# Kernel tuning notes

Measured on AMD Instinct MI355X. Metric: run time of the kernel, lower is better.

The kernel has to match this reference:

```python
import jax, jax.numpy as jnp
import numpy as np

P = 512       # input_shape
HD = 256      # hidden_dim
N = 65536     # number of samples
LAM1 = 1.0
LAM3 = 1.0


def setup_inputs() -> dict:
    key = jax.random.key(0)
    ks = jax.random.split(key, 12)
    def lin(kw, kb, out_d, in_d):
        lim = 1.0 / np.sqrt(in_d)
        W = jax.random.uniform(kw, (out_d, in_d), jnp.float32, -lim, lim)
        b = jax.random.uniform(kb, (out_d,), jnp.float32, -lim, lim)
        return W, b
    W1, b1 = lin(ks[0], ks[1], 200, P + HD)
    W12, b12 = lin(ks[2], ks[3], 100, 200)
    W13, b13 = lin(ks[4], ks[5], 100, 100)
    W2, b2 = lin(ks[6], ks[7], P, 100)
    return {
        "input": jax.random.normal(ks[8], (N, P), jnp.float32),
        "h": jax.random.normal(ks[9], (N, HD), jnp.float32),
        "W1": W1, "b1": b1, "W12": W12, "b12": b12,
        "W13": W13, "b13": b13, "W2": W2, "b2": b2,
        "idx0": 0, "idx1": N,
    }


def reference(input, h, W1, b1, W12, b12, W13, b13, W2, b2, idx0, idx1):
    n = input.shape[0]
    hs = h[idx0:idx1]                                   # [N, HD]
    x = jnp.concatenate([input, hs], axis=1)            # [N, P+HD]
    x = jax.nn.relu(x @ W1.T + b1)                      # dropout = identity (eval)
    x = jax.nn.relu(x @ W12.T + b12)
    x = jax.nn.relu(x @ W13.T + b13)
    f_x_h = x @ W2.T + b2                               # [N, P]
    mu = jnp.mean(hs, axis=0)                           # [HD]
    # S = mean_i <h_i, h_i> : vectorized sum-of-squares (replaces Python loop)
    S = jnp.mean(jnp.sum(hs * hs, axis=1))
    part0 = jnp.linalg.norm(f_x_h[:-1] - input[1:]) / (n - 1)
    part1 = LAM1 * jnp.sum(jnp.abs(mu)) / HD
    part2 = LAM1 * jnp.abs(S / HD - 1.0)
    part3 = LAM3 * jnp.mean(jnp.sum(jnp.abs(hs[1:] - hs[:-1]), axis=1)) / HD
    return (f_x_h, part0, part1, part2, part3)
```

## Files before the change

### kernel.cpp

```cpp
#include <hip/hip_runtime.h>

typedef __bf16 bf16;
typedef __bf16 bf16x8 __attribute__((ext_vector_type(8)));
typedef float f32x4 __attribute__((ext_vector_type(4)));

#define N_ROWS 65536

#define W1_E   159744
#define W12_E  25088
#define W13_E  14336
#define W2_E   65536
#define WP_TOTAL (W1_E + W12_E + W13_E + W2_E)
#define W12_OFF_B 319488
#define W13_OFF_B 369664
#define W2_OFF_B  398336
#define BP_OFF_BYTES (WP_TOTAL * 2)
#define BP_FLOATS 944
#define ACC_OFF_BYTES (BP_OFF_BYTES + BP_FLOATS * 4)
#define NCOPY 16
#define ACC_FLOATS (NCOPY * 256 + 3)
#define P0_IDX (NCOPY * 256)
#define S_IDX  (NCOPY * 256 + 1)
#define P3_IDX (NCOPY * 256 + 2)

__device__ inline int swz4(int r) { return (r ^ (r >> 2)) & 3; }

__global__ void pack_kernel(const float* __restrict__ W1, const float* __restrict__ b1,
                            const float* __restrict__ W12, const float* __restrict__ b12,
                            const float* __restrict__ W13, const float* __restrict__ b13,
                            const float* __restrict__ W2, const float* __restrict__ b2,
                            bf16* __restrict__ wp, float* __restrict__ bp) {
  int i = blockIdx.x * 256 + threadIdx.x;
  if (i < WP_TOTAL) {
    float v = 0.0f;
    if (i < W1_E) {
      int s = i / 6656, b = i - s * 6656;
      int r = b >> 5, w = b & 31;
      int k = s * 32 + (((w >> 3) ^ swz4(r)) << 3) + (w & 7);
      if (r < 200) v = W1[r * 768 + k];
    } else if (i < W1_E + W12_E) {
      int j = i - W1_E;
      int s = j / 3584, b = j - s * 3584;
      int r = b >> 5, w = b & 31;
      int k = s * 32 + (((w >> 3) ^ swz4(r)) << 3) + (w & 7);
      if (r < 100 && k < 200) v = W12[r * 200 + k];
    } else if (i < W1_E + W12_E + W13_E) {
      int j = i - (W1_E + W12_E);
      int s = j / 3584, b = j - s * 3584;
      int r = b >> 5, w = b & 31;
      int k = s * 32 + (((w >> 3) ^ swz4(r)) << 3) + (w & 7);
      if (r < 100 && k < 100) v = W13[r * 100 + k];
    } else {
      int j = i - (W1_E + W12_E + W13_E);
      int g = j >> 14, rest = j & 16383;
      int s = rest >> 12, b = rest & 4095;
      int r = b >> 5, w = b & 31;
      int o = g * 128 + r;
      int k = s * 32 + (((w >> 3) ^ swz4(r)) << 3) + (w & 7);
      if (k < 100) v = W2[o * 100 + k];
    }
    wp[i] = (bf16)v;
  } else {
    int j = i - WP_TOTAL;
    if (j < BP_FLOATS) {
      float v = 0.0f;
      if (j < 208)      { if (j < 200) v = b1[j]; }
      else if (j < 320) { int o = j - 208; if (o < 100) v = b12[o]; }
      else if (j < 432) { int o = j - 320; if (o < 100) v = b13[o]; }
      else              { v = b2[j - 432]; }
      bp[j] = v;
    }
  }
}

#define MFMA(a, b, c) __builtin_amdgcn_mfma_f32_16x16x32_bf16((a), (b), (c), 0, 0, 0)

template<int BYTES>
__device__ inline void stage(const char* __restrict__ src, bf16* __restrict__ dstw, int tid) {
  char* dst = (char*)dstw;
  const int off0 = (tid >> 6) * 1024 + (tid & 63) * 16;
  constexpr int NCH = (BYTES + 4095) / 4096;
#pragma unroll
  for (int j = 0; j < NCH; j++) {
    const int off = j * 4096 + off0;
    if ((BYTES & 4095) == 0 || off < BYTES)
      __builtin_amdgcn_global_load_lds(
          (const __attribute__((address_space(1))) void*)(src + off),
          (__attribute__((address_space(3))) void*)(dst + off),
          16, 0, 0);
  }
}

__global__ __launch_bounds__(256, 2) void mlp_main(
    const float* __restrict__ input, const float* __restrict__ h,
    const bf16* __restrict__ wp, const float* __restrict__ bp,
    float* __restrict__ out, float* __restrict__ p0_accum) {
  __shared__ __align__(16) bf16 acts[4][3712];
  __shared__ __align__(16) bf16 wbuf[2][6656];
  __shared__ float p0red[4];

  const int tid = threadIdx.x;
  const int lane = tid & 63;
  const int wave = tid >> 6;
  const int c16 = lane & 15;
  const int quad = lane >> 4;
  const int m0 = blockIdx.x * 64 + wave * 16;
  const int qs8 = (quad ^ swz4(c16)) * 8;

  const char* wpb = (const char*)wp;
  const float* b1p  = bp;
  const float* b12p = bp + 208;
  const float* b13p = bp + 320;
  const float* b2p  = bp + 432;

  bf16* actw = &acts[wave][0];

  f32x4 acc1[13];
#pragma unroll
  for (int t = 0; t < 13; t++) acc1[t] = (f32x4){0.f, 0.f, 0.f, 0.f};

  stage<13312>(wpb, wbuf[0], tid);
  __syncthreads();

  const float* arow = input + (size_t)(m0 + c16) * 512 + quad * 8;
  const float* hrow = h + (size_t)(m0 + c16) * 256 + quad * 8;
  f32x4 abuf[16];
  for (int kb = 0; kb < 3; kb++) {
#pragma unroll
    for (int b = 0; b < 8; b++) {
      const int kk = kb * 8 + b;
      const float* p = (kk < 16) ? (arow + kk * 32) : (hrow + (kk - 16) * 32);
      abuf[b * 2]     = *(const f32x4*)p;
      abuf[b * 2 + 1] = *(const f32x4*)(p + 4);
    }
#pragma unroll
    for (int b = 0; b < 8; b++) {
      const int ks = kb * 8 + b;
      if (ks + 1 < 24) stage<13312>(wpb + (ks + 1) * 13312, wbuf[(b + 1) & 1], tid);
      bf16x8 a;
#pragma unroll
      for (int q = 0; q < 4; q++) { a[q] = (bf16)abuf[b * 2][q]; a[4 + q] = (bf16)abuf[b * 2 + 1][q]; }
      const bf16* buf = wbuf[b & 1];
#pragma unroll
      for (int t = 0; t < 13; t++) {
        bf16x8 bb = *(const bf16x8*)(buf + (t * 16 + c16) * 32 + qs8);
        acc1[t] = MFMA(a, bb, acc1[t]);
      }
      __syncthreads();
    }
  }
#pragma unroll
  for (int t = 0; t < 13; t++) {
    const float bias = b1p[t * 16 + c16];
#pragma unroll
    for (int r = 0; r < 4; r++)
      actw[(quad * 4 + r) * 232 + t * 16 + c16] = (bf16)fmaxf(acc1[t][r] + bias, 0.0f);
  }
  for (int idx = lane; idx < 256; idx += 64)
    actw[(idx >> 4) * 232 + 208 + (idx & 15)] = (bf16)0.0f;

  f32x4 acc2[7];
#pragma unroll
  for (int t = 0; t < 7; t++) acc2[t] = (f32x4){0.f, 0.f, 0.f, 0.f};

  stage<7168>(wpb + W12_OFF_B, wbuf[0], tid);
  __syncthreads();
#pragma unroll
  for (int ks = 0; ks < 7; ks++) {
    if (ks + 1 < 7) stage<7168>(wpb + W12_OFF_B + (ks + 1) * 7168, wbuf[(ks + 1) & 1], tid);
    bf16x8 a = *(const bf16x8*)(actw + c16 * 232 + ks * 32 + quad * 8);
    const bf16* buf = wbuf[ks & 1];
#pragma unroll
    for (int t = 0; t < 7; t++) {
      bf16x8 bb = *(const bf16x8*)(buf + (t * 16 + c16) * 32 + qs8);
      acc2[t] = MFMA(a, bb, acc2[t]);
    }
    __syncthreads();
  }
#pragma unroll
  for (int t = 0; t < 7; t++) {
    const float bias = b12p[t * 16 + c16];
#pragma unroll
    for (int r = 0; r < 4; r++)
      actw[(quad * 4 + r) * 136 + t * 16 + c16] = (bf16)fmaxf(acc2[t][r] + bias, 0.0f);
  }
  for (int idx = lane; idx < 256; idx += 64)
    actw[(idx >> 4) * 136 + 112 + (idx & 15)] = (bf16)0.0f;

  f32x4 acc3[7];
#pragma unroll
  for (int t = 0; t < 7; t++) acc3[t] = (f32x4){0.f, 0.f, 0.f, 0.f};

  stage<7168>(wpb + W13_OFF_B, wbuf[0], tid);
  __syncthreads();
#pragma unroll
  for (int ks = 0; ks < 4; ks++) {
    if (ks + 1 < 4) stage<7168>(wpb + W13_OFF_B + (ks + 1) * 7168, wbuf[(ks + 1) & 1], tid);
    bf16x8 a = *(const bf16x8*)(actw + c16 * 136 + ks * 32 + quad * 8);
    const bf16* buf = wbuf[ks & 1];
#pragma unroll
    for (int t = 0; t < 7; t++) {
      bf16x8 bb = *(const bf16x8*)(buf + (t * 16 + c16) * 32 + qs8);
      acc3[t] = MFMA(a, bb, acc3[t]);
    }
    __syncthreads();
  }
#pragma unroll
  for (int t = 0; t < 7; t++) {
    const float bias = b13p[t * 16 + c16];
#pragma unroll
    for (int r = 0; r < 4; r++)
      actw[(quad * 4 + r) * 136 + t * 16 + c16] = (bf16)fmaxf(acc3[t][r] + bias, 0.0f);
  }
  for (int idx = lane; idx < 256; idx += 64)
    actw[(idx >> 4) * 136 + 112 + (idx & 15)] = (bf16)0.0f;

  float p0local = 0.0f;
  for (int g = 0; g < 4; g++) {
    f32x4 acc4[8];
#pragma unroll
    for (int t = 0; t < 8; t++) acc4[t] = (f32x4){0.f, 0.f, 0.f, 0.f};

    const char* Wg = wpb + W2_OFF_B + g * 32768;
    stage<8192>(Wg, wbuf[0], tid);
    __syncthreads();
#pragma unroll
    for (int ks = 0; ks < 4; ks++) {
      if (ks + 1 < 4) stage<8192>(Wg + (ks + 1) * 8192, wbuf[(ks + 1) & 1], tid);
      bf16x8 a = *(const bf16x8*)(actw + c16 * 136 + ks * 32 + quad * 8);
      const bf16* buf = wbuf[ks & 1];
#pragma unroll
      for (int t = 0; t < 8; t++) {
        bf16x8 bb = *(const bf16x8*)(buf + (t * 16 + c16) * 32 + qs8);
        acc4[t] = MFMA(a, bb, acc4[t]);
      }
      __syncthreads();
    }
#pragma unroll
    for (int t = 0; t < 8; t++) {
      const int o = g * 128 + t * 16 + c16;
      const float bias = b2p[o];
#pragma unroll
      for (int r = 0; r < 4; r++) {
        const int grow = m0 + quad * 4 + r;
        float v = acc4[t][r] + bias;
        out[(size_t)grow * 512 + o] = v;
        if (grow < N_ROWS - 1) {
          float d = v - input[(size_t)(grow + 1) * 512 + o];
          p0local += d * d;
        }
      }
    }
  }
#pragma unroll
  for (int off = 32; off > 0; off >>= 1) p0local += __shfl_down(p0local, off);
  if (lane == 0) p0red[wave] = p0local;
  __syncthreads();
  if (tid == 0) atomicAdd(p0_accum, p0red[0] + p0red[1] + p0red[2] + p0red[3]);
}

__global__ __launch_bounds__(256) void reduce_h(const float* __restrict__ h, float* __restrict__ acc) {
  __shared__ f32x4 cbuf[256];
  __shared__ float redS[256];
  __shared__ float redP[256];
  const int t = threadIdx.x;
  const int c = t & 63;
  const int rg = t >> 6;
  const int start = blockIdx.x * 256 + rg * 64;

  const float* base = h + (size_t)start * 256 + c * 4;
  f32x4 prev = *(const f32x4*)base;
  f32x4 csum = prev;
  f32x4 s2v = prev * prev;
  f32x4 p3v = (f32x4){0.f, 0.f, 0.f, 0.f};
#pragma unroll 8
  for (int r = 1; r < 64; r++) {
    f32x4 v = *(const f32x4*)(base + (size_t)r * 256);
    csum += v;
    s2v += v * v;
    f32x4 d = v - prev;
#pragma unroll
    for (int i = 0; i < 4; i++) p3v[i] += __builtin_fabsf(d[i]);
    prev = v;
  }
  if (start + 64 < N_ROWS) {
    f32x4 v = *(const f32x4*)(base + (size_t)64 * 256);
    f32x4 d = v - prev;
#pragma unroll
    for (int i = 0; i < 4; i++) p3v[i] += __builtin_fabsf(d[i]);
  }
  cbuf[t] = csum;
  redS[t] = s2v[0] + s2v[1] + s2v[2] + s2v[3];
  redP[t] = p3v[0] + p3v[1] + p3v[2] + p3v[3];
  __syncthreads();
  if (rg == 0) {
    f32x4 s = cbuf[c] + cbuf[c + 64] + cbuf[c + 128] + cbuf[c + 192];
    float* dst = acc + (blockIdx.x & (NCOPY - 1)) * 256 + 4 * c;
    atomicAdd(dst + 0, s[0]);
    atomicAdd(dst + 1, s[1]);
    atomicAdd(dst + 2, s[2]);
    atomicAdd(dst + 3, s[3]);
  }
  for (int st = 128; st > 0; st >>= 1) {
    if (t < st) { redS[t] += redS[t + st]; redP[t] += redP[t + st]; }
    __syncthreads();
  }
  if (t == 0) {
    atomicAdd(&acc[S_IDX], redS[0]);
    atomicAdd(&acc[P3_IDX], redP[0]);
  }
}

__global__ void finalize(const float* __restrict__ acc, float* __restrict__ out) {
  __shared__ float red[256];
  const int t = threadIdx.x;
  float s = 0.0f;
#pragma unroll
  for (int j = 0; j < NCOPY; j++) s += acc[j * 256 + t];
  red[t] = fabsf(s);
  __syncthreads();
  for (int st = 128; st > 0; st >>= 1) {
    if (t < st) red[t] += red[t + st];
    __syncthreads();
  }
  if (t == 0) {
    out[(size_t)N_ROWS * 512 + 0] = sqrtf(acc[P0_IDX]) / 65535.0f;
    out[(size_t)N_ROWS * 512 + 1] = red[0] / 65536.0f / 256.0f;
    out[(size_t)N_ROWS * 512 + 2] = fabsf(acc[S_IDX] / (65536.0f * 256.0f) - 1.0f);
    out[(size_t)N_ROWS * 512 + 3] = acc[P3_IDX] / (65535.0f * 256.0f);
  }
}

extern "C" void kernel_launch(void* const* d_in, const int* in_sizes, int n_in,
                              void* d_out, int out_size, void* d_ws, size_t ws_size,
                              hipStream_t stream) {
  const float* input = (const float*)d_in[0];
  const float* h   = (const float*)d_in[1];
  const float* W1  = (const float*)d_in[2];
  const float* b1  = (const float*)d_in[3];
  const float* W12 = (const float*)d_in[4];
  const float* b12 = (const float*)d_in[5];
  const float* W13 = (const float*)d_in[6];
  const float* b13 = (const float*)d_in[7];
  const float* W2  = (const float*)d_in[8];
  const float* b2  = (const float*)d_in[9];
  float* out = (float*)d_out;

  bf16* wp = (bf16*)d_ws;
  float* bp = (float*)((char*)d_ws + BP_OFF_BYTES);
  float* acc = (float*)((char*)d_ws + ACC_OFF_BYTES);

  hipMemsetAsync(acc, 0, ACC_FLOATS * sizeof(float), stream);
  pack_kernel<<<(WP_TOTAL + BP_FLOATS + 255) / 256, 256, 0, stream>>>(
      W1, b1, W12, b12, W13, b13, W2, b2, wp, bp);
  mlp_main<<<N_ROWS / 64, 256, 0, stream>>>(input, h, wp, bp, out, acc + P0_IDX);
  reduce_h<<<N_ROWS / 256, 256, 0, stream>>>(h, acc);
  finalize<<<1, 256, 0, stream>>>(acc, out);
}
```

Measured before the change: 412.9 us.

## Coalesce A-tile loads via LDS staging and widen h-reduction parallelism

In the MLP kernel, each wave now loads its 16 input/h rows with coalesced 128-column float4 reads, converts them to bf16, and writes them into a swizzled per-wave LDS buffer. MFMA operands are then read from that buffer, and the next chunk is prefetched into registers. This replaces the old per-lane strided 32-byte reads straight from global memory. The h statistics reduction now launches 8x more blocks, each covering 8 rows per thread, and the scalar S/P3 atomics are spread across 16 copies to cut contention. The cost is 16 KB of extra LDS per block, which may affect occupancy, plus more atomics overall.

```diff
diff --git a/kernel.cpp b/kernel.cpp
--- a/kernel.cpp
+++ b/kernel.cpp
@@ -1,6 +1,7 @@
 #include <hip/hip_runtime.h>
 
 typedef __bf16 bf16;
+typedef __bf16 bf16x4 __attribute__((ext_vector_type(4)));
 typedef __bf16 bf16x8 __attribute__((ext_vector_type(8)));
 typedef float f32x4 __attribute__((ext_vector_type(4)));
 
@@ -18,10 +19,10 @@
 #define BP_FLOATS 944
 #define ACC_OFF_BYTES (BP_OFF_BYTES + BP_FLOATS * 4)
 #define NCOPY 16
-#define ACC_FLOATS (NCOPY * 256 + 3)
 #define P0_IDX (NCOPY * 256)
-#define S_IDX  (NCOPY * 256 + 1)
-#define P3_IDX (NCOPY * 256 + 2)
+#define S_IDX0 (P0_IDX + 1)
+#define P3_IDX0 (S_IDX0 + NCOPY)
+#define ACC_FLOATS (P3_IDX0 + NCOPY)
 
 __device__ inline int swz4(int r) { return (r ^ (r >> 2)) & 3; }
 
@@ -97,6 +98,7 @@
     float* __restrict__ out, float* __restrict__ p0_accum) {
   __shared__ __align__(16) bf16 acts[4][3712];
   __shared__ __align__(16) bf16 wbuf[2][6656];
+  __shared__ __align__(16) bf16 abuf[4][2048];
   __shared__ float p0red[4];
 
   const int tid = threadIdx.x;
@@ -114,33 +116,51 @@
   const float* b2p  = bp + 432;
 
   bf16* actw = &acts[wave][0];
+  bf16* aw = &abuf[wave][0];
 
   f32x4 acc1[13];
 #pragma unroll
   for (int t = 0; t < 13; t++) acc1[t] = (f32x4){0.f, 0.f, 0.f, 0.f};
 
+  f32x4 ar[8];
+  auto loadA = [&](int kb) {
+#pragma unroll
+    for (int i = 0; i < 8; i++) {
+      const int row = 2 * i + (lane >> 5);
+      const int col = (lane & 31) * 4;
+      const float* src = (kb < 4)
+          ? (input + (size_t)(m0 + row) * 512 + kb * 128 + col)
+          : (h + (size_t)(m0 + row) * 256 + (kb - 4) * 128 + col);
+      ar[i] = *(const f32x4*)src;
+    }
+  };
+  auto writeA = [&]() {
+    const int kk = (lane & 31) >> 3;
+    const int q  = ((lane & 31) >> 1) & 3;
+    const int sub = (lane & 1) * 4;
+#pragma unroll
+    for (int i = 0; i < 8; i++) {
+      const int row = 2 * i + (lane >> 5);
+      bf16x4 cv;
+#pragma unroll
+      for (int c = 0; c < 4; c++) cv[c] = (bf16)ar[i][c];
+      *(bf16x4*)(aw + kk * 512 + row * 32 + ((q ^ swz4(row)) * 8) + sub) = cv;
+    }
+  };
+
   stage<13312>(wpb, wbuf[0], tid);
-  __syncthreads();
-
-  const float* arow = input + (size_t)(m0 + c16) * 512 + quad * 8;
-  const float* hrow = h + (size_t)(m0 + c16) * 256 + quad * 8;
-  f32x4 abuf[16];
-  for (int kb = 0; kb < 3; kb++) {
-#pragma unroll
-    for (int b = 0; b < 8; b++) {
-      const int kk = kb * 8 + b;
-      const float* p = (kk < 16) ? (arow + kk * 32) : (hrow + (kk - 16) * 32);
-      abuf[b * 2]     = *(const f32x4*)p;
-      abuf[b * 2 + 1] = *(const f32x4*)(p + 4);
-    }
-#pragma unroll
-    for (int b = 0; b < 8; b++) {
-      const int ks = kb * 8 + b;
-      if (ks + 1 < 24) stage<13312>(wpb + (ks + 1) * 13312, wbuf[(b + 1) & 1], tid);
-      bf16x8 a;
-#pragma unroll
-      for (int q = 0; q < 4; q++) { a[q] = (bf16)abuf[b * 2][q]; a[4 + q] = (bf16)abuf[b * 2 + 1][q]; }
-      const bf16* buf = wbuf[b & 1];
+  loadA(0);
+
+  for (int kb = 0; kb < 6; kb++) {
+    writeA();
+    __syncthreads();
+#pragma unroll
+    for (int j = 0; j < 4; j++) {
+      const int ks = kb * 4 + j;
+      if (j == 0 && kb + 1 < 6) loadA(kb + 1);
+      if (ks + 1 < 24) stage<13312>(wpb + (ks + 1) * 13312, wbuf[(ks + 1) & 1], tid);
+      bf16x8 a = *(const bf16x8*)(aw + j * 512 + c16 * 32 + qs8);
+      const bf16* buf = wbuf[ks & 1];
 #pragma unroll
       for (int t = 0; t < 13; t++) {
         bf16x8 bb = *(const bf16x8*)(buf + (t * 16 + c16) * 32 + qs8);
@@ -266,26 +286,23 @@
   const int t = threadIdx.x;
   const int c = t & 63;
   const int rg = t >> 6;
-  const int start = blockIdx.x * 256 + rg * 64;
+  const int start = blockIdx.x * 32 + rg * 8;
 
   const float* base = h + (size_t)start * 256 + c * 4;
-  f32x4 prev = *(const f32x4*)base;
-  f32x4 csum = prev;
-  f32x4 s2v = prev * prev;
-  f32x4 p3v = (f32x4){0.f, 0.f, 0.f, 0.f};
-#pragma unroll 8
-  for (int r = 1; r < 64; r++) {
-    f32x4 v = *(const f32x4*)(base + (size_t)r * 256);
-    csum += v;
-    s2v += v * v;
-    f32x4 d = v - prev;
-#pragma unroll
-    for (int i = 0; i < 4; i++) p3v[i] += __builtin_fabsf(d[i]);
-    prev = v;
-  }
-  if (start + 64 < N_ROWS) {
-    f32x4 v = *(const f32x4*)(base + (size_t)64 * 256);
-    f32x4 d = v - prev;
+  f32x4 v[9];
+#pragma unroll
+  for (int r = 0; r < 8; r++) v[r] = *(const f32x4*)(base + (size_t)r * 256);
+  if (start + 8 < N_ROWS) v[8] = *(const f32x4*)(base + (size_t)8 * 256);
+  else                    v[8] = v[7];
+
+  f32x4 csum = (f32x4){0.f, 0.f, 0.f, 0.f};
+  f32x4 s2v  = (f32x4){0.f, 0.f, 0.f, 0.f};
+  f32x4 p3v  = (f32x4){0.f, 0.f, 0.f, 0.f};
+#pragma unroll
+  for (int r = 0; r < 8; r++) {
+    csum += v[r];
+    s2v  += v[r] * v[r];
+    f32x4 d = v[r + 1] - v[r];
 #pragma unroll
     for (int i = 0; i < 4; i++) p3v[i] += __builtin_fabsf(d[i]);
   }
@@ -306,8 +323,8 @@
     __syncthreads();
   }
   if (t == 0) {
-    atomicAdd(&acc[S_IDX], redS[0]);
-    atomicAdd(&acc[P3_IDX], redP[0]);
+    atomicAdd(&acc[S_IDX0 + (blockIdx.x & (NCOPY - 1))], redS[0]);
+    atomicAdd(&acc[P3_IDX0 + (blockIdx.x & (NCOPY - 1))], redP[0]);
   }
 }
 
@@ -324,10 +341,13 @@
     __syncthreads();
   }
   if (t == 0) {
+    float Ssum = 0.f, Psum = 0.f;
+#pragma unroll
+    for (int j = 0; j < NCOPY; j++) { Ssum += acc[S_IDX0 + j]; Psum += acc[P3_IDX0 + j]; }
     out[(size_t)N_ROWS * 512 + 0] = sqrtf(acc[P0_IDX]) / 65535.0f;
     out[(size_t)N_ROWS * 512 + 1] = red[0] / 65536.0f / 256.0f;
-    out[(size_t)N_ROWS * 512 + 2] = fabsf(acc[S_IDX] / (65536.0f * 256.0f) - 1.0f);
-    out[(size_t)N_ROWS * 512 + 3] = acc[P3_IDX] / (65535.0f * 256.0f);
+    out[(size_t)N_ROWS * 512 + 2] = fabsf(Ssum / (65536.0f * 256.0f) - 1.0f);
+    out[(size_t)N_ROWS * 512 + 3] = Psum / (65535.0f * 256.0f);
   }
 }
 
@@ -354,6 +374,6 @@
   pack_kernel<<<(WP_TOTAL + BP_FLOATS + 255) / 256, 256, 0, stream>>>(
       W1, b1, W12, b12, W13, b13, W2, b2, wp, bp);
   mlp_main<<<N_ROWS / 64, 256, 0, stream>>>(input, h, wp, bp, out, acc + P0_IDX);
-  reduce_h<<<N_ROWS / 256, 256, 0, stream>>>(h, acc);
+  reduce_h<<<N_ROWS / 32, 256, 0, stream>>>(h, acc);
   finalize<<<1, 256, 0, stream>>>(acc, out);
 }
```

Measured after the change: 431.8 us. +4.6%, slower.
